# Optimization experiments

Hardware: AMD Instinct MI355X
Metric: run time of the kernel (lower is better)

Reference implementation:

```python
import jax, jax.numpy as jnp
import numpy as np

N = 50000
E = 1600000
D_IN = 128
D_OUT = 128


def setup_inputs() -> dict:
    key = jax.random.key(0)
    k1, k2, k3, k4, k5, k6 = jax.random.split(key, 6)
    row = jax.random.randint(k1, (E,), 0, N, dtype=jnp.int32)
    col = jax.random.randint(k2, (E,), 0, N, dtype=jnp.int32)
    vals = jax.random.uniform(k3, (E,), dtype=jnp.float32)
    features = jax.random.normal(k4, (N, D_IN), dtype=jnp.float32)
    weight = jax.random.normal(k5, (D_IN, D_OUT), dtype=jnp.float32)
    bias = jax.random.normal(k6, (D_OUT,), dtype=jnp.float32)
    return {"row": row, "col": col, "vals": vals, "features": features,
            "weight": weight, "bias": bias}


def reference(row, col, vals, features, weight, bias):
    # SpMM aggregation: out[i] = sum_j adj[i,j] * features[j]
    # adj given in COO: (row, col, vals)
    gathered = vals[:, None] * features[col]          # [E, D_IN]
    agg = jax.ops.segment_sum(gathered, row, num_segments=N)  # [N, D_IN]
    # dense feature transform + bias
    return agg @ weight + bias                        # [N, D_OUT]
```

## Files before the change

### kernel.cpp

```cpp
#include <hip/hip_runtime.h>
#include <hip/hip_bf16.h>


#define D 128
#define NREP 8
#define RPB 128
#define BCAP 5120
#define EPB 4096
#define NBMAX 512

typedef __attribute__((ext_vector_type(8))) short short8;
typedef __attribute__((ext_vector_type(4))) float f32x4;

__device__ __forceinline__ ushort bf16bits(float x) {
    return __hip_bfloat16_raw(__float2bfloat16(x)).x;
}

__global__ __launch_bounds__(256) void prep_k(const float* __restrict__ W,
                                              ushort* __restrict__ Wt,
                                              int* __restrict__ gcur, int NB) {
    const int idx = blockIdx.x * 256 + threadIdx.x;
    if (idx < D * D) {
        const int k = idx >> 7, c = idx & 127;
        Wt[c * D + k] = bf16bits(W[idx]);
    }
    if (idx < NB) gcur[idx] = 0;
}

__global__ __launch_bounds__(256) void fused_gemm_scatter_k(
    const float* __restrict__ F, const ushort* __restrict__ Wt,
    ushort* __restrict__ Gb, int nrows,
    const int* __restrict__ row, const int* __restrict__ col,
    const float* __restrict__ vals, int* __restrict__ gcur,
    uint2* __restrict__ pairs, int E, int NB, int GB) {
    __shared__ int hist[NBMAX];
    __shared__ int cur[NBMAX];

    if ((int)blockIdx.x < GB) {
        const int wave = threadIdx.x >> 6;
        const int lane = threadIdx.x & 63;
        const int r0 = (blockIdx.x * 8 + wave * 2) * 16;
        if (r0 >= nrows) return;
        const int lr = lane & 15;
        const int lg = lane >> 4;

        f32x4 acc0[8], acc1[8];
        #pragma unroll
        for (int c = 0; c < 8; ++c) {
            acc0[c] = (f32x4){0.f, 0.f, 0.f, 0.f};
            acc1[c] = (f32x4){0.f, 0.f, 0.f, 0.f};
        }

        int ar0 = r0 + lr;      if (ar0 >= nrows) ar0 = nrows - 1;
        int ar1 = r0 + 16 + lr; if (ar1 >= nrows) ar1 = nrows - 1;
        const float* __restrict__ a0p = F + (size_t)ar0 * D + lg * 8;
        const float* __restrict__ a1p = F + (size_t)ar1 * D + lg * 8;

        #pragma unroll
        for (int kk = 0; kk < 4; ++kk) {
            const float4 x0 = *(const float4*)(a0p + kk * 32);
            const float4 x1 = *(const float4*)(a0p + kk * 32 + 4);
            const float4 y0 = *(const float4*)(a1p + kk * 32);
            const float4 y1 = *(const float4*)(a1p + kk * 32 + 4);
            short8 af0, af1;
            af0[0] = (short)bf16bits(x0.x); af0[1] = (short)bf16bits(x0.y);
            af0[2] = (short)bf16bits(x0.z); af0[3] = (short)bf16bits(x0.w);
            af0[4] = (short)bf16bits(x1.x); af0[5] = (short)bf16bits(x1.y);
            af0[6] = (short)bf16bits(x1.z); af0[7] = (short)bf16bits(x1.w);
            af1[0] = (short)bf16bits(y0.x); af1[1] = (short)bf16bits(y0.y);
            af1[2] = (short)bf16bits(y0.z); af1[3] = (short)bf16bits(y0.w);
            af1[4] = (short)bf16bits(y1.x); af1[5] = (short)bf16bits(y1.y);
            af1[6] = (short)bf16bits(y1.z); af1[7] = (short)bf16bits(y1.w);
            #pragma unroll
            for (int c = 0; c < 8; ++c) {
                const short8 bf = *(const short8*)(Wt + (size_t)(c * 16 + lr) * D + kk * 32 + lg * 8);
                acc0[c] = __builtin_amdgcn_mfma_f32_16x16x32_bf16(af0, bf, acc0[c], 0, 0, 0);
                acc1[c] = __builtin_amdgcn_mfma_f32_16x16x32_bf16(af1, bf, acc1[c], 0, 0, 0);
            }
        }

        uint* __restrict__ g32 = (uint*)Gb;
        #pragma unroll
        for (int i = 0; i < 4; ++i) {
            const int rr0 = r0 + 4 * lg + i;
            if (rr0 < nrows) {
                #pragma unroll
                for (int c = 0; c < 4; ++c)
                    g32[(size_t)rr0 * 64 + c * 16 + lr] =
                        (uint)bf16bits(acc0[c][i]) | ((uint)bf16bits(acc0[c + 4][i]) << 16);
            }
            const int rr1 = r0 + 16 + 4 * lg + i;
            if (rr1 < nrows) {
                #pragma unroll
                for (int c = 0; c < 4; ++c)
                    g32[(size_t)rr1 * 64 + c * 16 + lr] =
                        (uint)bf16bits(acc1[c][i]) | ((uint)bf16bits(acc1[c + 4][i]) << 16);
            }
        }
        return;
    }

    const int t = threadIdx.x;
    for (int i = t; i < NB; i += 256) hist[i] = 0;
    __syncthreads();

    const int e0 = ((int)blockIdx.x - GB) * EPB;
    const int e1 = min(e0 + EPB, E);

    for (int e = e0 + t; e < e1; e += 256)
        atomicAdd(&hist[row[e] >> 7], 1);
    __syncthreads();

    for (int i = t; i < NB; i += 256) {
        const int h = hist[i];
        cur[i] = (h > 0) ? atomicAdd(&gcur[i], h) : 0;
    }
    __syncthreads();

    for (int e = e0 + t; e < e1; e += 256) {
        const int r = row[e];
        const int b = r >> 7;
        const int slot = atomicAdd(&cur[b], 1);
        if (slot < BCAP)
            pairs[(size_t)b * BCAP + slot] =
                make_uint2(((uint)col[e] << 16) | bf16bits(vals[e]), (uint)(r & (RPB - 1)));
    }
}

__global__ __launch_bounds__(512) void bucket_to_csr_k(
    uint2* __restrict__ bpairs, const int* __restrict__ gcur,
    int* __restrict__ offs, int* __restrict__ counts, int N) {
    __shared__ uint2 ents[BCAP];
    __shared__ int hist[RPB];
    __shared__ int roff[RPB];
    __shared__ int cur[RPB];
    const int t = threadIdx.x, b = blockIdx.x;
    if (t < RPB) hist[t] = 0;
    __syncthreads();

    int cnt = gcur[b];
    if (cnt > BCAP) cnt = BCAP;
    const uint2* __restrict__ in = bpairs + (size_t)b * BCAP;
    for (int j = t; j < cnt; j += 512) {
        const uint2 e = in[j];
        ents[j] = e;
        atomicAdd(&hist[e.y], 1);
    }
    __syncthreads();

    if (t < RPB) roff[t] = hist[t];
    __syncthreads();
    for (int off = 1; off < RPB; off <<= 1) {
        const int x = (t < RPB && t >= off) ? roff[t - off] : 0;
        __syncthreads();
        if (t < RPB) roff[t] += x;
        __syncthreads();
    }
    if (t < RPB) {
        const int ex = roff[t] - hist[t];
        roff[t] = ex;
        cur[t] = 0;
        const int rg = b * RPB + t;
        if (rg < N) {
            offs[rg] = b * 2 * BCAP + ex;
            counts[rg] = hist[t];
        }
    }
    __syncthreads();

    uint* __restrict__ outv = (uint*)bpairs + (size_t)b * 2 * BCAP;
    for (int j = t; j < cnt; j += 512) {
        const uint2 e = ents[j];
        const int k = atomicAdd(&cur[e.y], 1);
        outv[roff[e.y] + k] = e.x;
    }
}

__global__ __launch_bounds__(256) void csr_gather_bf16_k(
    const uint* __restrict__ pairs, const int* __restrict__ offs,
    const int* __restrict__ counts, const uint* __restrict__ Gu,
    const float* __restrict__ bias, float* __restrict__ out, int n) {
    const int wid = (blockIdx.x * 256 + threadIdx.x) >> 6;
    if (wid >= n) return;
    const int lane = threadIdx.x & 63;

    float2 acc = make_float2(bias[lane], bias[64 + lane]);
    const int start = offs[wid];
    const int cnt = counts[wid];
    const uint* __restrict__ pp = pairs + start;

    int j = 0;
    for (; j + 7 < cnt; j += 8) {
        uint p[8], g[8];
        #pragma unroll
        for (int k = 0; k < 8; ++k) p[k] = pp[j + k];
        #pragma unroll
        for (int k = 0; k < 8; ++k) g[k] = Gu[(size_t)(p[k] >> 16) * (D / 2) + lane];
        #pragma unroll
        for (int k = 0; k < 8; ++k) {
            const float v = __uint_as_float(p[k] << 16);
            acc.x += v * __uint_as_float(g[k] << 16);
            acc.y += v * __uint_as_float(g[k] & 0xffff0000u);
        }
    }
    for (; j + 3 < cnt; j += 4) {
        uint p[4], g[4];
        #pragma unroll
        for (int k = 0; k < 4; ++k) p[k] = pp[j + k];
        #pragma unroll
        for (int k = 0; k < 4; ++k) g[k] = Gu[(size_t)(p[k] >> 16) * (D / 2) + lane];
        #pragma unroll
        for (int k = 0; k < 4; ++k) {
            const float v = __uint_as_float(p[k] << 16);
            acc.x += v * __uint_as_float(g[k] << 16);
            acc.y += v * __uint_as_float(g[k] & 0xffff0000u);
        }
    }
    for (; j < cnt; ++j) {
        const uint p = pp[j];
        const uint g = Gu[(size_t)(p >> 16) * (D / 2) + lane];
        const float v = __uint_as_float(p << 16);
        acc.x += v * __uint_as_float(g << 16);
        acc.y += v * __uint_as_float(g & 0xffff0000u);
    }
    out[(size_t)wid * D + lane] = acc.x;
    out[(size_t)wid * D + 64 + lane] = acc.y;
}

__global__ __launch_bounds__(256) void transposeW_k(const float* __restrict__ W,
                                                    ushort* __restrict__ Wt) {
    const int idx = blockIdx.x * 256 + threadIdx.x;
    const int k = idx >> 7, c = idx & 127;
    Wt[c * D + k] = bf16bits(W[idx]);
}

__global__ __launch_bounds__(256) void gemm_mfma_k(
    const float* __restrict__ F, const ushort* __restrict__ Wt,
    ushort* __restrict__ Gb, int nrows) {
    const int wave = threadIdx.x >> 6;
    const int lane = threadIdx.x & 63;
    const int row0 = (blockIdx.x * 4 + wave) * 16;
    if (row0 >= nrows) return;
    const int lr = lane & 15;
    const int lg = lane >> 4;

    f32x4 acc[8];
    #pragma unroll
    for (int c = 0; c < 8; ++c) acc[c] = (f32x4){0.f, 0.f, 0.f, 0.f};

    int arow_idx = row0 + lr;
    if (arow_idx >= nrows) arow_idx = nrows - 1;
    const float* __restrict__ arow = F + (size_t)arow_idx * D + lg * 8;

    #pragma unroll
    for (int kk = 0; kk < 4; ++kk) {
        const float4 a0 = *(const float4*)(arow + kk * 32);
        const float4 a1 = *(const float4*)(arow + kk * 32 + 4);
        short8 af;
        af[0] = (short)bf16bits(a0.x); af[1] = (short)bf16bits(a0.y);
        af[2] = (short)bf16bits(a0.z); af[3] = (short)bf16bits(a0.w);
        af[4] = (short)bf16bits(a1.x); af[5] = (short)bf16bits(a1.y);
        af[6] = (short)bf16bits(a1.z); af[7] = (short)bf16bits(a1.w);
        #pragma unroll
        for (int c = 0; c < 8; ++c) {
            const short8 bf = *(const short8*)(Wt + (size_t)(c * 16 + lr) * D + kk * 32 + lg * 8);
            acc[c] = __builtin_amdgcn_mfma_f32_16x16x32_bf16(af, bf, acc[c], 0, 0, 0);
        }
    }

    ushort* __restrict__ gout = Gb + (size_t)row0 * D;
    #pragma unroll
    for (int i = 0; i < 4; ++i) {
        const int r = 4 * lg + i;
        if (row0 + r < nrows) {
            #pragma unroll
            for (int c = 0; c < 8; ++c) {
                const int j = c * 16 + lr;
                const int pos = (c < 4) ? (2 * j) : (2 * (j - 64) + 1);
                gout[(size_t)r * D + pos] = bf16bits(acc[c][i]);
            }
        }
    }
}

__global__ __launch_bounds__(256) void hist_rank_rep_k(const int* __restrict__ row,
                                                       int* __restrict__ cntrep,
                                                       ushort* __restrict__ rank,
                                                       int E, int N) {
    const int e = blockIdx.x * 256 + threadIdx.x;
    if (e >= E) return;
    const int rep = blockIdx.x & (NREP - 1);
    rank[e] = (ushort)atomicAdd(&cntrep[rep * N + row[e]], 1);
}

__global__ __launch_bounds__(256) void repbase_k(int* __restrict__ cntrep,
                                                 int* __restrict__ tot, int N) {
    const int r = blockIdx.x * 256 + threadIdx.x;
    if (r >= N) return;
    int s = 0;
    #pragma unroll
    for (int rep = 0; rep < NREP; ++rep) {
        const int v = cntrep[rep * N + r];
        cntrep[rep * N + r] = s;
        s += v;
    }
    tot[r] = s;
}

__global__ __launch_bounds__(256) void scan_blocks_k(const int* __restrict__ counts,
                                                     int* __restrict__ offs,
                                                     int* __restrict__ blockSums, int n) {
    __shared__ int s[256];
    const int t = threadIdx.x;
    const int i = blockIdx.x * 256 + t;
    const int v = (i < n) ? counts[i] : 0;
    s[t] = v;
    __syncthreads();
    for (int off = 1; off < 256; off <<= 1) {
        int x = (t >= off) ? s[t - off] : 0;
        __syncthreads();
        s[t] += x;
        __syncthreads();
    }
    if (i < n) offs[i] = s[t] - v;
    if (t == 255) blockSums[blockIdx.x] = s[255];
}

__global__ __launch_bounds__(256) void scan_top_k(int* __restrict__ blockSums, int nb) {
    __shared__ int s[256];
    const int t = threadIdx.x;
    const int v = (t < nb) ? blockSums[t] : 0;
    s[t] = v;
    __syncthreads();
    for (int off = 1; off < 256; off <<= 1) {
        int x = (t >= off) ? s[t - off] : 0;
        __syncthreads();
        s[t] += x;
        __syncthreads();
    }
    if (t < nb) blockSums[t] = s[t] - v;
}

__global__ __launch_bounds__(256) void scan_add_k(int* __restrict__ offs,
                                                  const int* __restrict__ blockSums,
                                                  int n) {
    int i = blockIdx.x * 256 + threadIdx.x;
    if (i < n) offs[i] += blockSums[blockIdx.x];
}

__global__ __launch_bounds__(256) void fill_pack_k(const int* __restrict__ row,
                                                   const int* __restrict__ col,
                                                   const float* __restrict__ vals,
                                                   const int* __restrict__ offs,
                                                   const ushort* __restrict__ rank,
                                                   const int* __restrict__ cntrep,
                                                   uint* __restrict__ pairs, int E, int N) {
    const int e = blockIdx.x * 256 + threadIdx.x;
    if (e >= E) return;
    const int r = row[e];
    const int rep = (e >> 8) & (NREP - 1);
    const int pos = offs[r] + cntrep[rep * N + r] + (int)rank[e];
    pairs[pos] = ((uint)col[e] << 16) | bf16bits(vals[e]);
}

#define ROWS_PER_BLOCK 64
__global__ __launch_bounds__(256) void gemm_f32_k(
    const float* __restrict__ A, const float* __restrict__ W,
    const float* __restrict__ bias, float* __restrict__ out, int nrows) {
    __shared__ float Wlds[D * D];
    {
        const float4* W4 = (const float4*)W;
        float4* Wl4 = (float4*)Wlds;
        #pragma unroll
        for (int i = 0; i < (D * D / 4) / 256; ++i)
            Wl4[threadIdx.x + i * 256] = W4[threadIdx.x + i * 256];
    }
    __syncthreads();
    const int lane = threadIdx.x & 31;
    const int rsub = threadIdx.x >> 5;
    const float4 b = ((const float4*)bias)[lane];
    const int rowBase = blockIdx.x * ROWS_PER_BLOCK;
    for (int rr = rsub; rr < ROWS_PER_BLOCK; rr += 8) {
        const int r = rowBase + rr;
        if (r >= nrows) break;
        const float* __restrict__ arow = A + (size_t)r * D;
        float4 acc = b;
        #pragma unroll 4
        for (int k4 = 0; k4 < D / 4; ++k4) {
            const float4 a = ((const float4*)arow)[k4];
            const int k = k4 * 4;
            const float4 w0 = ((const float4*)(Wlds + (k + 0) * D))[lane];
            const float4 w1 = ((const float4*)(Wlds + (k + 1) * D))[lane];
            const float4 w2 = ((const float4*)(Wlds + (k + 2) * D))[lane];
            const float4 w3 = ((const float4*)(Wlds + (k + 3) * D))[lane];
            acc.x += a.x * w0.x + a.y * w1.x + a.z * w2.x + a.w * w3.x;
            acc.y += a.x * w0.y + a.y * w1.y + a.z * w2.y + a.w * w3.y;
            acc.z += a.x * w0.z + a.y * w1.z + a.z * w2.z + a.w * w3.z;
            acc.w += a.x * w0.w + a.y * w1.w + a.z * w2.w + a.w * w3.w;
        }
        ((float4*)(out + (size_t)r * D))[lane] = acc;
    }
}

__global__ __launch_bounds__(256) void spmm_scatter(
    const int* __restrict__ row, const int* __restrict__ col,
    const float* __restrict__ vals, const float* __restrict__ feat,
    float* __restrict__ agg, int E) {
    int gid = blockIdx.x * 256 + threadIdx.x;
    int e = gid >> 5;
    if (e >= E) return;
    int lane = gid & 31;
    int r = row[e];
    int c = col[e];
    float v = vals[e];
    float4 f = ((const float4*)(feat + (size_t)c * D))[lane];
    float* dst = agg + (size_t)r * D + lane * 4;
    atomicAdd(dst + 0, v * f.x);
    atomicAdd(dst + 1, v * f.y);
    atomicAdd(dst + 2, v * f.z);
    atomicAdd(dst + 3, v * f.w);
}

extern "C" void kernel_launch(void* const* d_in, const int* in_sizes, int n_in,
                              void* d_out, int out_size, void* d_ws, size_t ws_size,
                              hipStream_t stream) {
    const int* row = (const int*)d_in[0];
    const int* col = (const int*)d_in[1];
    const float* vals = (const float*)d_in[2];
    const float* feat = (const float*)d_in[3];
    const float* W = (const float*)d_in[4];
    const float* bias = (const float*)d_in[5];
    float* out = (float*)d_out;

    const int E = in_sizes[0];
    const int N = out_size / D;
    const int NB = (N + RPB - 1) / RPB;

    const size_t Gb_bytes = (size_t)N * D * sizeof(ushort);
    const size_t wt_bytes = (size_t)D * D * sizeof(ushort);
    const size_t cnt_bytes = (size_t)N * sizeof(int);

    const size_t bpairs_bytes = (size_t)NB * BCAP * sizeof(uint2);
    const size_t gcur_bytes = ((size_t)NB * sizeof(int) + 255) & ~(size_t)255;
    const size_t need_bucket = Gb_bytes + bpairs_bytes + gcur_bytes +
                               2 * cnt_bytes + wt_bytes;

    const size_t pairs_bytes = (size_t)E * sizeof(uint);
    const size_t rank_bytes = ((size_t)E * sizeof(ushort) + 3) & ~(size_t)3;
    const size_t cntrep_bytes = (size_t)NREP * N * sizeof(int);
    const size_t bs_bytes = 256 * sizeof(int);
    const size_t need_compact = Gb_bytes + pairs_bytes + rank_bytes + cntrep_bytes +
                                2 * cnt_bytes + bs_bytes + wt_bytes;

    if (ws_size >= need_bucket && N <= 65536 && NB <= NBMAX) {
        char* p = (char*)d_ws;
        ushort* Gb = (ushort*)p;   p += Gb_bytes;
        uint2* bpairs = (uint2*)p; p += bpairs_bytes;
        int* gcur = (int*)p;       p += gcur_bytes;
        int* offs = (int*)p;       p += cnt_bytes;
        int* counts = (int*)p;     p += cnt_bytes;
        ushort* Wt = (ushort*)p;   p += wt_bytes;

        const int GB = (N + 127) / 128;
        const int SB = (E + EPB - 1) / EPB;

        prep_k<<<(D * D + 255) / 256, 256, 0, stream>>>(W, Wt, gcur, NB);
        fused_gemm_scatter_k<<<GB + SB, 256, 0, stream>>>(
            feat, Wt, Gb, N, row, col, vals, gcur, bpairs, E, NB, GB);
        bucket_to_csr_k<<<NB, 512, 0, stream>>>(bpairs, gcur, offs, counts, N);
        csr_gather_bf16_k<<<(N * 64 + 255) / 256, 256, 0, stream>>>(
            (const uint*)bpairs, offs, counts, (const uint*)Gb, bias, out, N);
    } else if (ws_size >= need_compact && N <= 65536) {
        char* p = (char*)d_ws;
        ushort* Gb = (ushort*)p;   p += Gb_bytes;
        uint* pairs = (uint*)p;    p += pairs_bytes;
        ushort* rank = (ushort*)p; p += rank_bytes;
        int* cntrep = (int*)p;     p += cntrep_bytes;
        int* tot = (int*)p;        p += cnt_bytes;
        int* offs = (int*)p;       p += cnt_bytes;
        int* blockSums = (int*)p;  p += bs_bytes;
        ushort* Wt = (ushort*)p;   p += wt_bytes;

        const int nScanBlocks = (N + 255) / 256;

        transposeW_k<<<(D * D) / 256, 256, 0, stream>>>(W, Wt);
        gemm_mfma_k<<<(N + 63) / 64, 256, 0, stream>>>(feat, Wt, Gb, N);

        hipMemsetAsync(cntrep, 0, cntrep_bytes, stream);
        hist_rank_rep_k<<<(E + 255) / 256, 256, 0, stream>>>(row, cntrep, rank, E, N);
        repbase_k<<<(N + 255) / 256, 256, 0, stream>>>(cntrep, tot, N);
        scan_blocks_k<<<nScanBlocks, 256, 0, stream>>>(tot, offs, blockSums, N);
        scan_top_k<<<1, 256, 0, stream>>>(blockSums, nScanBlocks);
        scan_add_k<<<nScanBlocks, 256, 0, stream>>>(offs, blockSums, N);
        fill_pack_k<<<(E + 255) / 256, 256, 0, stream>>>(row, col, vals, offs, rank,
                                                         cntrep, pairs, E, N);
        csr_gather_bf16_k<<<(N * 64 + 255) / 256, 256, 0, stream>>>(
            pairs, offs, tot, (const uint*)Gb, bias, out, N);
    } else {
        float* agg = (float*)d_ws;
        hipMemsetAsync(agg, 0, (size_t)N * D * sizeof(float), stream);
        long long threads = (long long)E * 32;
        spmm_scatter<<<(int)((threads + 255) / 256), 256, 0, stream>>>(
            row, col, vals, feat, agg, E);
        gemm_f32_k<<<(N + ROWS_PER_BLOCK - 1) / ROWS_PER_BLOCK, 256, 0, stream>>>(
            agg, W, bias, out, N);
    }
}
```

Measured before the change: 205.9 us.

## Split gather into four column passes with 8 lanes per row

Replaces the one-wave-per-row CSR gather with a kernel that handles 8 rows per wave, each row served by 8 lanes loading uint2 (4 bf16) per edge. The 128 output columns are covered in four separate column passes launched as one grid. Each pass touches only a quarter of the G rows, which is meant to improve cache locality and raise memory-level parallelism per wave. In exchange, the pair lists and offsets are re-read four times. The fused GEMM/scatter kernel now puts scatter blocks first in the grid so they are scheduled before GEMM blocks, and the old gather's 8-way unroll is reduced to 4, though that kernel is no longer launched.

```diff
diff --git a/kernel.cpp b/kernel.cpp
--- a/kernel.cpp
+++ b/kernel.cpp
@@ -32,14 +32,15 @@
     ushort* __restrict__ Gb, int nrows,
     const int* __restrict__ row, const int* __restrict__ col,
     const float* __restrict__ vals, int* __restrict__ gcur,
-    uint2* __restrict__ pairs, int E, int NB, int GB) {
+    uint2* __restrict__ pairs, int E, int NB, int SB) {
     __shared__ int hist[NBMAX];
     __shared__ int cur[NBMAX];
 
-    if ((int)blockIdx.x < GB) {
+    if ((int)blockIdx.x >= SB) {
+        const int gb = (int)blockIdx.x - SB;
         const int wave = threadIdx.x >> 6;
         const int lane = threadIdx.x & 63;
-        const int r0 = (blockIdx.x * 8 + wave * 2) * 16;
+        const int r0 = (gb * 8 + wave * 2) * 16;
         if (r0 >= nrows) return;
         const int lr = lane & 15;
         const int lg = lane >> 4;
@@ -104,7 +105,7 @@
     for (int i = t; i < NB; i += 256) hist[i] = 0;
     __syncthreads();
 
-    const int e0 = ((int)blockIdx.x - GB) * EPB;
+    const int e0 = (int)blockIdx.x * EPB;
     const int e1 = min(e0 + EPB, E);
 
     for (int e = e0 + t; e < e1; e += 256)
@@ -176,6 +177,73 @@
     }
 }
 
+__global__ __launch_bounds__(256) void gather4p_k(
+    const uint* __restrict__ pairs, const int* __restrict__ offs,
+    const int* __restrict__ counts, const uint* __restrict__ Gu,
+    const float* __restrict__ bias, float* __restrict__ out, int n, int nbp) {
+    const int wave = threadIdx.x >> 6;
+    const int lane = threadIdx.x & 63;
+    const int grp = lane >> 3;
+    const int u = lane & 7;
+    const int pass = blockIdx.x / nbp;
+    const int r = (blockIdx.x % nbp) * 32 + wave * 8 + grp;
+    if (r >= n) return;
+
+    const int base = pass * 16 + 2 * u;
+    float2 accA = make_float2(0.f, 0.f);
+    float2 accB = make_float2(0.f, 0.f);
+
+    const int start = offs[r];
+    const int cnt = counts[r];
+    const uint* __restrict__ pp = pairs + start;
+
+    int j = 0;
+    for (; j + 3 < cnt; j += 4) {
+        const uint p0 = pp[j + 0];
+        const uint p1 = pp[j + 1];
+        const uint p2 = pp[j + 2];
+        const uint p3 = pp[j + 3];
+        const uint2 g0 = *(const uint2*)(Gu + ((size_t)(p0 >> 16) * 64 + base));
+        const uint2 g1 = *(const uint2*)(Gu + ((size_t)(p1 >> 16) * 64 + base));
+        const uint2 g2 = *(const uint2*)(Gu + ((size_t)(p2 >> 16) * 64 + base));
+        const uint2 g3 = *(const uint2*)(Gu + ((size_t)(p3 >> 16) * 64 + base));
+        const float v0 = __uint_as_float(p0 << 16);
+        const float v1 = __uint_as_float(p1 << 16);
+        const float v2 = __uint_as_float(p2 << 16);
+        const float v3 = __uint_as_float(p3 << 16);
+        accA.x += v0 * __uint_as_float(g0.x << 16);
+        accB.x += v0 * __uint_as_float(g0.x & 0xffff0000u);
+        accA.y += v0 * __uint_as_float(g0.y << 16);
+        accB.y += v0 * __uint_as_float(g0.y & 0xffff0000u);
+        accA.x += v1 * __uint_as_float(g1.x << 16);
+        accB.x += v1 * __uint_as_float(g1.x & 0xffff0000u);
+        accA.y += v1 * __uint_as_float(g1.y << 16);
+        accB.y += v1 * __uint_as_float(g1.y & 0xffff0000u);
+        accA.x += v2 * __uint_as_float(g2.x << 16);
+        accB.x += v2 * __uint_as_float(g2.x & 0xffff0000u);
+        accA.y += v2 * __uint_as_float(g2.y << 16);
+        accB.y += v2 * __uint_as_float(g2.y & 0xffff0000u);
+        accA.x += v3 * __uint_as_float(g3.x << 16);
+        accB.x += v3 * __uint_as_float(g3.x & 0xffff0000u);
+        accA.y += v3 * __uint_as_float(g3.y << 16);
+        accB.y += v3 * __uint_as_float(g3.y & 0xffff0000u);
+    }
+    for (; j < cnt; ++j) {
+        const uint p = pp[j];
+        const uint2 g = *(const uint2*)(Gu + ((size_t)(p >> 16) * 64 + base));
+        const float v = __uint_as_float(p << 16);
+        accA.x += v * __uint_as_float(g.x << 16);
+        accB.x += v * __uint_as_float(g.x & 0xffff0000u);
+        accA.y += v * __uint_as_float(g.y << 16);
+        accB.y += v * __uint_as_float(g.y & 0xffff0000u);
+    }
+
+    const float2 bA = *(const float2*)(bias + base);
+    const float2 bB = *(const float2*)(bias + 64 + base);
+    *(float2*)(out + (size_t)r * D + base) = make_float2(accA.x + bA.x, accA.y + bA.y);
+    *(float2*)(out + (size_t)r * D + 64 + base) = make_float2(accB.x + bB.x, accB.y + bB.y);
+}
+
 __global__ __launch_bounds__(256) void csr_gather_bf16_k(
     const uint* __restrict__ pairs, const int* __restrict__ offs,
     const int* __restrict__ counts, const uint* __restrict__ Gu,
@@ -190,31 +258,27 @@
     const uint* __restrict__ pp = pairs + start;
 
     int j = 0;
-    for (; j + 7 < cnt; j += 8) {
-        uint p[8], g[8];
-        #pragma unroll
-        for (int k = 0; k < 8; ++k) p[k] = pp[j + k];
-        #pragma unroll
-        for (int k = 0; k < 8; ++k) g[k] = Gu[(size_t)(p[k] >> 16) * (D / 2) + lane];
-        #pragma unroll
-        for (int k = 0; k < 8; ++k) {
-            const float v = __uint_as_float(p[k] << 16);
-            acc.x += v * __uint_as_float(g[k] << 16);
-            acc.y += v * __uint_as_float(g[k] & 0xffff0000u);
-        }
-    }
     for (; j + 3 < cnt; j += 4) {
-        uint p[4], g[4];
-        #pragma unroll
-        for (int k = 0; k < 4; ++k) p[k] = pp[j + k];
-        #pragma unroll
-        for (int k = 0; k < 4; ++k) g[k] = Gu[(size_t)(p[k] >> 16) * (D / 2) + lane];
-        #pragma unroll
-        for (int k = 0; k < 4; ++k) {
-            const float v = __uint_as_float(p[k] << 16);
-            acc.x += v * __uint_as_float(g[k] << 16);
-            acc.y += v * __uint_as_float(g[k] & 0xffff0000u);
-        }
+        const uint p0 = pp[j + 0];
+        const uint p1 = pp[j + 1];
+        const uint p2 = pp[j + 2];
+        const uint p3 = pp[j + 3];
+        const uint g0 = Gu[(size_t)(p0 >> 16) * (D / 2) + lane];
+        const uint g1 = Gu[(size_t)(p1 >> 16) * (D / 2) + lane];
+        const uint g2 = Gu[(size_t)(p2 >> 16) * (D / 2) + lane];
+        const uint g3 = Gu[(size_t)(p3 >> 16) * (D / 2) + lane];
+        const float v0 = __uint_as_float(p0 << 16);
+        const float v1 = __uint_as_float(p1 << 16);
+        const float v2 = __uint_as_float(p2 << 16);
+        const float v3 = __uint_as_float(p3 << 16);
+        acc.x += v0 * __uint_as_float(g0 << 16);
+        acc.y += v0 * __uint_as_float(g0 & 0xffff0000u);
+        acc.x += v1 * __uint_as_float(g1 << 16);
+        acc.y += v1 * __uint_as_float(g1 & 0xffff0000u);
+        acc.x += v2 * __uint_as_float(g2 << 16);
+        acc.y += v2 * __uint_as_float(g2 & 0xffff0000u);
+        acc.x += v3 * __uint_as_float(g3 << 16);
+        acc.y += v3 * __uint_as_float(g3 & 0xffff0000u);
     }
     for (; j < cnt; ++j) {
         const uint p = pp[j];
@@ -463,13 +527,14 @@
 
         const int GB = (N + 127) / 128;
         const int SB = (E + EPB - 1) / EPB;
+        const int nbp = (N + 31) / 32;
 
         prep_k<<<(D * D + 255) / 256, 256, 0, stream>>>(W, Wt, gcur, NB);
-        fused_gemm_scatter_k<<<GB + SB, 256, 0, stream>>>(
-            feat, Wt, Gb, N, row, col, vals, gcur, bpairs, E, NB, GB);
+        fused_gemm_scatter_k<<<SB + GB, 256, 0, stream>>>(
+            feat, Wt, Gb, N, row, col, vals, gcur, bpairs, E, NB, SB);
         bucket_to_csr_k<<<NB, 512, 0, stream>>>(bpairs, gcur, offs, counts, N);
-        csr_gather_bf16_k<<<(N * 64 + 255) / 256, 256, 0, stream>>>(
-            (const uint*)bpairs, offs, counts, (const uint*)Gb, bias, out, N);
+        gather4p_k<<<4 * nbp, 256, 0, stream>>>(
+            (const uint*)bpairs, offs, counts, (const uint*)Gb, bias, out, N, nbp);
     } else if (ws_size >= need_compact && N <= 65536) {
         char* p = (char*)d_ws;
         ushort* Gb = (ushort*)p;   p += Gb_bytes;
```

New measurement: 227.8 us. +10.6%, slower.
